# Kernel tuning notes

Measured on AMD Instinct MI355X. Metric: run time of the kernel, lower is better.

The kernel has to match this reference:

```python
import jax, jax.numpy as jnp
import numpy as np

B, T, V, C, NB, NOPS = 8, 2048, 4096, 128, 64, 8

_NONLIN = [
    lambda h: h,
    jax.nn.relu,
    lambda h: jax.nn.gelu(h, approximate=False),
    lambda h: jnp.square(h),
    lambda h: -h,
    jnp.abs,
    jnp.tanh,
    jax.nn.sigmoid,
]


def setup_inputs() -> dict:
    key = jax.random.key(0)
    ks = jax.random.split(key, 6)
    s = 0.02
    return {
        "x": jax.random.normal(ks[0], (B, T, V), dtype=jnp.float32),
        "basis": jax.random.normal(ks[1], (V, 2 * NB), dtype=jnp.float32),
        "read_coeffs": jax.random.normal(ks[2], (C, 2 * NB), dtype=jnp.float32) * s,
        "write_coeffs": jax.random.normal(ks[3], (C, 2 * NB), dtype=jnp.float32) * s,
        "op_logits": jnp.zeros((NOPS,), dtype=jnp.float32),
        "op_weights": jax.random.normal(ks[4], (NOPS, C, C), dtype=jnp.float32) * s,
        "op_biases": jnp.zeros((NOPS, C), dtype=jnp.float32),
        "out_scale": jnp.float32(0.1),
    }


def op_bank(values, op_logits, op_weights, op_biases):
    # values: (B, T, C); soft mixture of 8 small channel transforms
    w = jax.nn.softmax(op_logits)  # (n_ops,)
    result = jnp.zeros_like(values)
    for i in range(NOPS):
        h = values @ op_weights[i] + op_biases[i]
        h = _NONLIN[i % len(_NONLIN)](h)
        result = result + w[i] * h
    return result


def reference(x, basis, read_coeffs, write_coeffs, op_logits, op_weights, op_biases, out_scale):
    # READ: Fourier soft addressing over V registers, normalized over registers (axis 0)
    read_w = jax.nn.softmax(basis @ read_coeffs.T, axis=0)  # (V, C)
    values = x @ read_w  # (B, T, C)
    # SELECT OP + APPLY
    values = op_bank(values, op_logits, op_weights, op_biases)
    # WRITE: unnormalized Fourier addressing back to registers
    write_w = basis @ write_coeffs.T  # (V, C)
    return (values @ write_w.T) * out_scale  # (B, T, V)
```

## Files before the change

### kernel.cpp

```cpp
#include <hip/hip_runtime.h>
#include <math.h>

#define M_TOT 16384
#define V_DIM 4096
#define C_DIM 128

typedef __bf16 bf16;
typedef __bf16 bf16x8 __attribute__((ext_vector_type(8)));
typedef float f32x4 __attribute__((ext_vector_type(4)));

__device__ inline f32x4 zero4() { f32x4 z; z[0]=0.f; z[1]=0.f; z[2]=0.f; z[3]=0.f; return z; }

__device__ inline bf16 f2bf(float f) {
  union { float f; unsigned u; } a; a.f = f;
  unsigned r = (a.u + 0x7FFFu + ((a.u >> 16) & 1u)) >> 16;
  union { unsigned short s; bf16 b; } o; o.s = (unsigned short)r;
  return o.b;
}

__device__ inline bf16x8 cvt8(float4 a, float4 b) {
  bf16x8 r;
  r[0]=f2bf(a.x); r[1]=f2bf(a.y); r[2]=f2bf(a.z); r[3]=f2bf(a.w);
  r[4]=f2bf(b.x); r[5]=f2bf(b.y); r[6]=f2bf(b.z); r[7]=f2bf(b.w);
  return r;
}

__global__ __launch_bounds__(256) void k_read(const float* __restrict__ basis,
                                              const float* __restrict__ rc,
                                              bf16* __restrict__ RT) {
  const int c = blockIdx.x;
  const int t = threadIdx.x;
  __shared__ __align__(16) float coeff[128];
  __shared__ float logits[4096];
  __shared__ float red[256];
  if (t < 128) coeff[t] = rc[c * 128 + t];
  __syncthreads();
  float lmax = -3.0e38f;
  for (int v = t; v < V_DIM; v += 256) {
    const float4* br = (const float4*)(basis + v * 128);
    const float4* cr = (const float4*)coeff;
    float s = 0.f;
#pragma unroll 8
    for (int k = 0; k < 32; k++) {
      float4 b4 = br[k]; float4 c4 = cr[k];
      s += b4.x * c4.x; s += b4.y * c4.y; s += b4.z * c4.z; s += b4.w * c4.w;
    }
    logits[v] = s;
    lmax = fmaxf(lmax, s);
  }
  red[t] = lmax;
  __syncthreads();
  for (int off = 128; off > 0; off >>= 1) {
    if (t < off) red[t] = fmaxf(red[t], red[t + off]);
    __syncthreads();
  }
  const float gmax = red[0];
  __syncthreads();
  float lsum = 0.f;
  for (int v = t; v < V_DIM; v += 256) {
    float e = __expf(logits[v] - gmax);
    logits[v] = e;
    lsum += e;
  }
  red[t] = lsum;
  __syncthreads();
  for (int off = 128; off > 0; off >>= 1) {
    if (t < off) red[t] += red[t + off];
    __syncthreads();
  }
  const float inv = 1.f / red[0];
  for (int v = t; v < V_DIM; v += 256)
    RT[c * V_DIM + v] = f2bf(logits[v] * inv);
}

__global__ __launch_bounds__(128) void k_write(const float* __restrict__ basis,
                                               const float* __restrict__ wc,
                                               bf16* __restrict__ W2) {
  const int v = blockIdx.x;
  const int c = threadIdx.x;
  __shared__ __align__(16) float brow[128];
  brow[c] = basis[v * 128 + c];
  __syncthreads();
  const float4* cr = (const float4*)(wc + c * 128);
  const float4* br = (const float4*)brow;
  float s = 0.f;
#pragma unroll 8
  for (int k = 0; k < 32; k++) {
    float4 a = br[k], b = cr[k];
    s += a.x * b.x; s += a.y * b.y; s += a.z * b.z; s += a.w * b.w;
  }
  W2[v * 128 + c] = f2bf(s);
}

__global__ __launch_bounds__(256) void k_ops(const float* __restrict__ opw,
                                             bf16* __restrict__ WTO) {
  int idx = blockIdx.x * 256 + threadIdx.x;
  int i = idx >> 14, rem = idx & 16383, n = rem >> 7, k = rem & 127;
  WTO[idx] = f2bf(opw[(i << 14) + k * 128 + n]);
}

__global__ __launch_bounds__(256) void k_gemm1(const float* __restrict__ x,
                                               const bf16* __restrict__ RT,
                                               bf16* __restrict__ val) {
  __shared__ __align__(16) bf16 Asm[64][72];
  __shared__ __align__(16) bf16 Bsm[128][72];
  const int t = threadIdx.x;
  const int m0 = blockIdx.x * 64;
  const int lane = t & 63, wave = t >> 6;
  const int fm = lane & 15, quad = lane >> 4;

  f32x4 acc[8];
#pragma unroll
  for (int i = 0; i < 8; i++) acc[i] = zero4();

  const int ar = t >> 2, ac = (t & 3) * 16;
  const int br = t >> 1, bc = (t & 1) * 32;
  const float* xp = x + (size_t)(m0 + ar) * V_DIM + ac;
  const bf16* bp = RT + br * V_DIM + bc;

  for (int k0 = 0; k0 < V_DIM; k0 += 64) {
    float4 a0 = *(const float4*)(xp + k0);
    float4 a1 = *(const float4*)(xp + k0 + 4);
    float4 a2 = *(const float4*)(xp + k0 + 8);
    float4 a3 = *(const float4*)(xp + k0 + 12);
    uint4 b0 = *(const uint4*)(bp + k0);
    uint4 b1 = *(const uint4*)(bp + k0 + 8);
    uint4 b2 = *(const uint4*)(bp + k0 + 16);
    uint4 b3 = *(const uint4*)(bp + k0 + 24);
    __syncthreads();
    *(bf16x8*)&Asm[ar][ac]     = cvt8(a0, a1);
    *(bf16x8*)&Asm[ar][ac + 8] = cvt8(a2, a3);
    *(uint4*)&Bsm[br][bc]      = b0;
    *(uint4*)&Bsm[br][bc + 8]  = b1;
    *(uint4*)&Bsm[br][bc + 16] = b2;
    *(uint4*)&Bsm[br][bc + 24] = b3;
    __syncthreads();
    bf16x8 af0 = *(const bf16x8*)&Asm[wave * 16 + fm][quad * 8];
    bf16x8 af1 = *(const bf16x8*)&Asm[wave * 16 + fm][32 + quad * 8];
#pragma unroll
    for (int nt = 0; nt < 8; nt++) {
      bf16x8 bf0 = *(const bf16x8*)&Bsm[nt * 16 + fm][quad * 8];
      bf16x8 bf1 = *(const bf16x8*)&Bsm[nt * 16 + fm][32 + quad * 8];
      acc[nt] = __builtin_amdgcn_mfma_f32_16x16x32_bf16(af0, bf0, acc[nt], 0, 0, 0);
      acc[nt] = __builtin_amdgcn_mfma_f32_16x16x32_bf16(af1, bf1, acc[nt], 0, 0, 0);
    }
  }
#pragma unroll
  for (int nt = 0; nt < 8; nt++)
#pragma unroll
    for (int r = 0; r < 4; r++) {
      int row = m0 + wave * 16 + quad * 4 + r;
      val[row * 128 + nt * 16 + fm] = f2bf(acc[nt][r]);
    }
}

__device__ inline float apply_nonlin(int i, float v) {
  switch (i) {
    case 0: return v;
    case 1: return fmaxf(v, 0.f);
    case 2: return 0.5f * v * (1.f + erff(v * 0.70710678118654752f));
    case 3: return v * v;
    case 4: return -v;
    case 5: return fabsf(v);
    case 6: return tanhf(v);
    default: return 1.f / (1.f + __expf(-v));
  }
}

__global__ __launch_bounds__(256) void k_opbank(const bf16* __restrict__ val,
                                                const bf16* __restrict__ WTO,
                                                const float* __restrict__ op_logits,
                                                const float* __restrict__ op_biases,
                                                bf16* __restrict__ val2) {
  __shared__ __align__(16) bf16 Asm[64][136];
  __shared__ __align__(16) bf16 Bsm[128][136];
  const int t = threadIdx.x;
  const int m0 = blockIdx.x * 64;
  const int lane = t & 63, wave = t >> 6;
  const int fm = lane & 15, quad = lane >> 4;

  float w[8];
  {
    float lm = -3.0e38f;
#pragma unroll
    for (int i = 0; i < 8; i++) { w[i] = op_logits[i]; lm = fmaxf(lm, w[i]); }
    float s = 0.f;
#pragma unroll
    for (int i = 0; i < 8; i++) { w[i] = __expf(w[i] - lm); s += w[i]; }
    float inv = 1.f / s;
#pragma unroll
    for (int i = 0; i < 8; i++) w[i] *= inv;
  }

  {
    const int row = t >> 2, off = (t & 3) * 32;
    const uint4* p = (const uint4*)(val + (m0 + row) * 128 + off);
    uint4 q0 = p[0], q1 = p[1], q2 = p[2], q3 = p[3];
    uint4* d = (uint4*)&Asm[row][off];
    d[0] = q0; d[1] = q1; d[2] = q2; d[3] = q3;
  }
  __syncthreads();
  bf16x8 af[4];
#pragma unroll
  for (int kk = 0; kk < 4; kk++)
    af[kk] = *(const bf16x8*)&Asm[wave * 16 + fm][kk * 32 + quad * 8];

  f32x4 res[8];
#pragma unroll
  for (int nt = 0; nt < 8; nt++) res[nt] = zero4();

  const int brow = t >> 1, boff = (t & 1) * 64;
  for (int i = 0; i < 8; i++) {
    __syncthreads();
    {
      const uint4* p = (const uint4*)(WTO + i * 16384 + brow * 128 + boff);
      uint4* d = (uint4*)&Bsm[brow][boff];
#pragma unroll
      for (int j = 0; j < 8; j++) d[j] = p[j];
    }
    __syncthreads();
#pragma unroll
    for (int nt = 0; nt < 8; nt++) {
      f32x4 h = zero4();
#pragma unroll
      for (int kk = 0; kk < 4; kk++) {
        bf16x8 bfr = *(const bf16x8*)&Bsm[nt * 16 + fm][kk * 32 + quad * 8];
        h = __builtin_amdgcn_mfma_f32_16x16x32_bf16(af[kk], bfr, h, 0, 0, 0);
      }
      float bias = op_biases[i * 128 + nt * 16 + fm];
#pragma unroll
      for (int r = 0; r < 4; r++) {
        float vv = h[r] + bias;
        res[nt][r] += w[i] * apply_nonlin(i, vv);
      }
    }
  }
#pragma unroll
  for (int nt = 0; nt < 8; nt++)
#pragma unroll
    for (int r = 0; r < 4; r++) {
      int row = m0 + wave * 16 + quad * 4 + r;
      val2[row * 128 + nt * 16 + fm] = f2bf(res[nt][r]);
    }
}

__global__ __launch_bounds__(256) void k_gemm2(const bf16* __restrict__ val2,
                                               const bf16* __restrict__ W2,
                                               const float* __restrict__ p_scale,
                                               float* __restrict__ out) {
  __shared__ __align__(16) bf16 Asm[64][136];
  __shared__ __align__(16) bf16 Bsm[128][136];
  const int t = threadIdx.x;
  const int m0 = (blockIdx.x >> 5) * 64;
  const int n0 = (blockIdx.x & 31) * 128;
  const int lane = t & 63, wave = t >> 6;
  const int fm = lane & 15, quad = lane >> 4;

  {
    const int row = t >> 2, off = (t & 3) * 32;
    const uint4* p = (const uint4*)(val2 + (m0 + row) * 128 + off);
    uint4* d = (uint4*)&Asm[row][off];
#pragma unroll
    for (int j = 0; j < 4; j++) d[j] = p[j];
  }
  {
    const int row = t >> 1, off = (t & 1) * 64;
    const uint4* p = (const uint4*)(W2 + (n0 + row) * 128 + off);
    uint4* d = (uint4*)&Bsm[row][off];
#pragma unroll
    for (int j = 0; j < 8; j++) d[j] = p[j];
  }
  __syncthreads();

  const float scale = *p_scale;
  bf16x8 af[4];
#pragma unroll
  for (int kk = 0; kk < 4; kk++)
    af[kk] = *(const bf16x8*)&Asm[wave * 16 + fm][kk * 32 + quad * 8];

#pragma unroll
  for (int nt = 0; nt < 8; nt++) {
    f32x4 acc = zero4();
#pragma unroll
    for (int kk = 0; kk < 4; kk++) {
      bf16x8 bfr = *(const bf16x8*)&Bsm[nt * 16 + fm][kk * 32 + quad * 8];
      acc = __builtin_amdgcn_mfma_f32_16x16x32_bf16(af[kk], bfr, acc, 0, 0, 0);
    }
#pragma unroll
    for (int r = 0; r < 4; r++) {
      int row = m0 + wave * 16 + quad * 4 + r;
      out[(size_t)row * V_DIM + n0 + nt * 16 + fm] = acc[r] * scale;
    }
  }
}

extern "C" void kernel_launch(void* const* d_in, const int* in_sizes, int n_in,
                              void* d_out, int out_size, void* d_ws, size_t ws_size,
                              hipStream_t stream) {
  const float* x      = (const float*)d_in[0];
  const float* basis  = (const float*)d_in[1];
  const float* rc     = (const float*)d_in[2];
  const float* wc     = (const float*)d_in[3];
  const float* oplog  = (const float*)d_in[4];
  const float* opw    = (const float*)d_in[5];
  const float* opb    = (const float*)d_in[6];
  const float* oscale = (const float*)d_in[7];
  float* out = (float*)d_out;
  char* ws = (char*)d_ws;

  bf16* RT   = (bf16*)(ws);
  bf16* W2   = (bf16*)(ws + (1u << 20));
  bf16* WTO  = (bf16*)(ws + (2u << 20));
  bf16* VAL  = (bf16*)(ws + (2u << 20) + (1u << 19));
  bf16* VAL2 = (bf16*)(ws + (2u << 20) + (1u << 19) + (4u << 20));

  k_read <<<C_DIM, 256, 0, stream>>>(basis, rc, RT);
  k_write<<<V_DIM, 128, 0, stream>>>(basis, wc, W2);
  k_ops  <<<512, 256, 0, stream>>>(opw, WTO);
  k_gemm1<<<M_TOT / 64, 256, 0, stream>>>(x, RT, VAL);
  k_opbank<<<M_TOT / 64, 256, 0, stream>>>(VAL, WTO, oplog, opb, VAL2);
  k_gemm2<<<(M_TOT / 64) * (V_DIM / 128), 256, 0, stream>>>(VAL2, W2, oscale, out);
}
```

Baseline: 653.3 us.

## Use MFMA for addressing matmuls, split-K gemm1, and stage gemm2 stores through LDS

Replaces the scalar read/write addressing kernels with MFMA-based GEMMs plus a separate register-resident softmax. gemm1 becomes split-K over 4 chunks for 4x more blocks, and the opbank kernel sums the partials, using 32-row tiles to double its block count. gemm2 reorders blocks to walk M fastest and writes output through LDS so the global stores are coalesced float4. This costs extra partial-sum traffic and one more bf16 rounding of the partial results.

```diff
diff --git a/kernel.cpp b/kernel.cpp
--- a/kernel.cpp
+++ b/kernel.cpp
@@ -25,29 +25,71 @@
   return r;
 }
 
-__global__ __launch_bounds__(256) void k_read(const float* __restrict__ basis,
-                                              const float* __restrict__ rc,
-                                              bf16* __restrict__ RT) {
-  const int c = blockIdx.x;
+__global__ __launch_bounds__(256) void k_logits(const float* __restrict__ basis,
+                                                const float* __restrict__ rc,
+                                                float* __restrict__ LT) {
+  __shared__ __align__(16) bf16 Asm[128][136];
+  __shared__ __align__(16) bf16 Bsm[128][136];
   const int t = threadIdx.x;
-  __shared__ __align__(16) float coeff[128];
-  __shared__ float logits[4096];
+  const int v0 = blockIdx.x * 128;
+  const int lane = t & 63, wave = t >> 6, fm = lane & 15, quad = lane >> 4;
+
+  {
+    const int row = t >> 1, c0 = (t & 1) * 64;
+    const float4* p = (const float4*)(rc + row * 128 + c0);
+    bf16x8* d = (bf16x8*)&Asm[row][c0];
+#pragma unroll
+    for (int j = 0; j < 8; j++) { float4 a = p[2*j], b = p[2*j+1]; d[j] = cvt8(a, b); }
+  }
+  {
+    const int row = t >> 1, c0 = (t & 1) * 64;
+    const float4* p = (const float4*)(basis + (size_t)(v0 + row) * 128 + c0);
+    bf16x8* d = (bf16x8*)&Bsm[row][c0];
+#pragma unroll
+    for (int j = 0; j < 8; j++) { float4 a = p[2*j], b = p[2*j+1]; d[j] = cvt8(a, b); }
+  }
+  __syncthreads();
+
+  f32x4 acc[2][8];
+#pragma unroll
+  for (int m = 0; m < 2; m++)
+#pragma unroll
+    for (int n = 0; n < 8; n++) acc[m][n] = zero4();
+
+#pragma unroll
+  for (int kk = 0; kk < 4; kk++) {
+    bf16x8 af[2];
+#pragma unroll
+    for (int m = 0; m < 2; m++)
+      af[m] = *(const bf16x8*)&Asm[wave * 32 + m * 16 + fm][kk * 32 + quad * 8];
+#pragma unroll
+    for (int nt = 0; nt < 8; nt++) {
+      bf16x8 bfr = *(const bf16x8*)&Bsm[nt * 16 + fm][kk * 32 + quad * 8];
+#pragma unroll
+      for (int m = 0; m < 2; m++)
+        acc[m][nt] = __builtin_amdgcn_mfma_f32_16x16x32_bf16(af[m], bfr, acc[m][nt], 0, 0, 0);
+    }
+  }
+#pragma unroll
+  for (int m = 0; m < 2; m++)
+#pragma unroll
+    for (int nt = 0; nt < 8; nt++)
+#pragma unroll
+      for (int r = 0; r < 4; r++) {
+        int c = wave * 32 + m * 16 + quad * 4 + r;
+        LT[(size_t)c * V_DIM + v0 + nt * 16 + fm] = acc[m][nt][r];
+      }
+}
+
+__global__ __launch_bounds__(256) void k_softmax(const float* __restrict__ LT,
+                                                 bf16* __restrict__ RT) {
+  const int c = blockIdx.x, t = threadIdx.x;
   __shared__ float red[256];
-  if (t < 128) coeff[t] = rc[c * 128 + t];
-  __syncthreads();
+  const float* row = LT + (size_t)c * V_DIM;
+  float e[16];
   float lmax = -3.0e38f;
-  for (int v = t; v < V_DIM; v += 256) {
-    const float4* br = (const float4*)(basis + v * 128);
-    const float4* cr = (const float4*)coeff;
-    float s = 0.f;
-#pragma unroll 8
-    for (int k = 0; k < 32; k++) {
-      float4 b4 = br[k]; float4 c4 = cr[k];
-      s += b4.x * c4.x; s += b4.y * c4.y; s += b4.z * c4.z; s += b4.w * c4.w;
-    }
-    logits[v] = s;
-    lmax = fmaxf(lmax, s);
-  }
+#pragma unroll
+  for (int j = 0; j < 16; j++) { e[j] = row[t + 256 * j]; lmax = fmaxf(lmax, e[j]); }
   red[t] = lmax;
   __syncthreads();
   for (int off = 128; off > 0; off >>= 1) {
@@ -57,11 +99,8 @@
   const float gmax = red[0];
   __syncthreads();
   float lsum = 0.f;
-  for (int v = t; v < V_DIM; v += 256) {
-    float e = __expf(logits[v] - gmax);
-    logits[v] = e;
-    lsum += e;
-  }
+#pragma unroll
+  for (int j = 0; j < 16; j++) { e[j] = __expf(e[j] - gmax); lsum += e[j]; }
   red[t] = lsum;
   __syncthreads();
   for (int off = 128; off > 0; off >>= 1) {
@@ -69,27 +108,55 @@
     __syncthreads();
   }
   const float inv = 1.f / red[0];
-  for (int v = t; v < V_DIM; v += 256)
-    RT[c * V_DIM + v] = f2bf(logits[v] * inv);
-}
-
-__global__ __launch_bounds__(128) void k_write(const float* __restrict__ basis,
-                                               const float* __restrict__ wc,
-                                               bf16* __restrict__ W2) {
-  const int v = blockIdx.x;
-  const int c = threadIdx.x;
-  __shared__ __align__(16) float brow[128];
-  brow[c] = basis[v * 128 + c];
-  __syncthreads();
-  const float4* cr = (const float4*)(wc + c * 128);
-  const float4* br = (const float4*)brow;
-  float s = 0.f;
-#pragma unroll 8
-  for (int k = 0; k < 32; k++) {
-    float4 a = br[k], b = cr[k];
-    s += a.x * b.x; s += a.y * b.y; s += a.z * b.z; s += a.w * b.w;
-  }
-  W2[v * 128 + c] = f2bf(s);
+#pragma unroll
+  for (int j = 0; j < 16; j++)
+    RT[(size_t)c * V_DIM + t + 256 * j] = f2bf(e[j] * inv);
+}
+
+__global__ __launch_bounds__(256) void k_w2(const float* __restrict__ basis,
+                                            const float* __restrict__ wc,
+                                            bf16* __restrict__ W2) {
+  __shared__ __align__(16) bf16 Asm[64][136];
+  __shared__ __align__(16) bf16 Bsm[128][136];
+  const int t = threadIdx.x;
+  const int v0 = blockIdx.x * 64;
+  const int lane = t & 63, wave = t >> 6, fm = lane & 15, quad = lane >> 4;
+
+  {
+    const int row = t >> 2, c0 = (t & 3) * 32;
+    const float4* p = (const float4*)(basis + (size_t)(v0 + row) * 128 + c0);
+    bf16x8* d = (bf16x8*)&Asm[row][c0];
+#pragma unroll
+    for (int j = 0; j < 4; j++) { float4 a = p[2*j], b = p[2*j+1]; d[j] = cvt8(a, b); }
+  }
+  {
+    const int row = t >> 1, c0 = (t & 1) * 64;
+    const float4* p = (const float4*)(wc + row * 128 + c0);
+    bf16x8* d = (bf16x8*)&Bsm[row][c0];
+#pragma unroll
+    for (int j = 0; j < 8; j++) { float4 a = p[2*j], b = p[2*j+1]; d[j] = cvt8(a, b); }
+  }
+  __syncthreads();
+
+  f32x4 acc[8];
+#pragma unroll
+  for (int n = 0; n < 8; n++) acc[n] = zero4();
+#pragma unroll
+  for (int kk = 0; kk < 4; kk++) {
+    bf16x8 af = *(const bf16x8*)&Asm[wave * 16 + fm][kk * 32 + quad * 8];
+#pragma unroll
+    for (int nt = 0; nt < 8; nt++) {
+      bf16x8 bfr = *(const bf16x8*)&Bsm[nt * 16 + fm][kk * 32 + quad * 8];
+      acc[nt] = __builtin_amdgcn_mfma_f32_16x16x32_bf16(af, bfr, acc[nt], 0, 0, 0);
+    }
+  }
+#pragma unroll
+  for (int nt = 0; nt < 8; nt++)
+#pragma unroll
+    for (int r = 0; r < 4; r++) {
+      int v = v0 + wave * 16 + quad * 4 + r;
+      W2[v * 128 + nt * 16 + fm] = f2bf(acc[nt][r]);
+    }
 }
 
 __global__ __launch_bounds__(256) void k_ops(const float* __restrict__ opw,
@@ -101,11 +168,12 @@
 
 __global__ __launch_bounds__(256) void k_gemm1(const float* __restrict__ x,
                                                const bf16* __restrict__ RT,
-                                               bf16* __restrict__ val) {
+                                               bf16* __restrict__ PART) {
   __shared__ __align__(16) bf16 Asm[64][72];
   __shared__ __align__(16) bf16 Bsm[128][72];
   const int t = threadIdx.x;
-  const int m0 = blockIdx.x * 64;
+  const int kc = blockIdx.x & 3;
+  const int m0 = (blockIdx.x >> 2) * 64;
   const int lane = t & 63, wave = t >> 6;
   const int fm = lane & 15, quad = lane >> 4;
 
@@ -116,9 +184,10 @@
   const int ar = t >> 2, ac = (t & 3) * 16;
   const int br = t >> 1, bc = (t & 1) * 32;
   const float* xp = x + (size_t)(m0 + ar) * V_DIM + ac;
-  const bf16* bp = RT + br * V_DIM + bc;
-
-  for (int k0 = 0; k0 < V_DIM; k0 += 64) {
+  const bf16* bp = RT + (size_t)br * V_DIM + bc;
+  const int kbeg = kc * 1024, kend = kbeg + 1024;
+
+  for (int k0 = kbeg; k0 < kend; k0 += 64) {
     float4 a0 = *(const float4*)(xp + k0);
     float4 a1 = *(const float4*)(xp + k0 + 4);
     float4 a2 = *(const float4*)(xp + k0 + 8);
@@ -145,12 +214,13 @@
       acc[nt] = __builtin_amdgcn_mfma_f32_16x16x32_bf16(af1, bf1, acc[nt], 0, 0, 0);
     }
   }
+  bf16* po = PART + (size_t)kc * (M_TOT * C_DIM);
 #pragma unroll
   for (int nt = 0; nt < 8; nt++)
 #pragma unroll
     for (int r = 0; r < 4; r++) {
       int row = m0 + wave * 16 + quad * 4 + r;
-      val[row * 128 + nt * 16 + fm] = f2bf(acc[nt][r]);
+      po[row * 128 + nt * 16 + fm] = f2bf(acc[nt][r]);
     }
 }
 
@@ -167,17 +237,18 @@
   }
 }
 
-__global__ __launch_bounds__(256) void k_opbank(const bf16* __restrict__ val,
+__global__ __launch_bounds__(256) void k_opbank(const bf16* __restrict__ PART,
                                                 const bf16* __restrict__ WTO,
                                                 const float* __restrict__ op_logits,
                                                 const float* __restrict__ op_biases,
                                                 bf16* __restrict__ val2) {
-  __shared__ __align__(16) bf16 Asm[64][136];
+  __shared__ __align__(16) bf16 Asm[32][136];
   __shared__ __align__(16) bf16 Bsm[128][136];
   const int t = threadIdx.x;
-  const int m0 = blockIdx.x * 64;
+  const int m0 = blockIdx.x * 32;
   const int lane = t & 63, wave = t >> 6;
   const int fm = lane & 15, quad = lane >> 4;
+  const int mf = wave & 1, nh = wave >> 1;
 
   float w[8];
   {
@@ -193,21 +264,33 @@
   }
 
   {
-    const int row = t >> 2, off = (t & 3) * 32;
-    const uint4* p = (const uint4*)(val + (m0 + row) * 128 + off);
-    uint4 q0 = p[0], q1 = p[1], q2 = p[2], q3 = p[3];
-    uint4* d = (uint4*)&Asm[row][off];
-    d[0] = q0; d[1] = q1; d[2] = q2; d[3] = q3;
-  }
-  __syncthreads();
+    const int row = t >> 3, c0 = (t & 7) * 16;
+    float accA[16];
+#pragma unroll
+    for (int j = 0; j < 16; j++) accA[j] = 0.f;
+#pragma unroll
+    for (int p = 0; p < 4; p++) {
+      const bf16x8* q = (const bf16x8*)(PART + (size_t)p * (M_TOT * C_DIM) + (m0 + row) * 128 + c0);
+      bf16x8 u0 = q[0], u1 = q[1];
+#pragma unroll
+      for (int j = 0; j < 8; j++) { accA[j] += (float)u0[j]; accA[8 + j] += (float)u1[j]; }
+    }
+    bf16x8 o0, o1;
+#pragma unroll
+    for (int j = 0; j < 8; j++) { o0[j] = f2bf(accA[j]); o1[j] = f2bf(accA[8 + j]); }
+    *(bf16x8*)&Asm[row][c0] = o0;
+    *(bf16x8*)&Asm[row][c0 + 8] = o1;
+  }
+  __syncthreads();
+
   bf16x8 af[4];
 #pragma unroll
   for (int kk = 0; kk < 4; kk++)
-    af[kk] = *(const bf16x8*)&Asm[wave * 16 + fm][kk * 32 + quad * 8];
-
-  f32x4 res[8];
-#pragma unroll
-  for (int nt = 0; nt < 8; nt++) res[nt] = zero4();
+    af[kk] = *(const bf16x8*)&Asm[mf * 16 + fm][kk * 32 + quad * 8];
+
+  f32x4 res[4];
+#pragma unroll
+  for (int j = 0; j < 4; j++) res[j] = zero4();
 
   const int brow = t >> 1, boff = (t & 1) * 64;
   for (int i = 0; i < 8; i++) {
@@ -220,7 +303,8 @@
     }
     __syncthreads();
 #pragma unroll
-    for (int nt = 0; nt < 8; nt++) {
+    for (int j = 0; j < 4; j++) {
+      const int nt = nh * 4 + j;
       f32x4 h = zero4();
 #pragma unroll
       for (int kk = 0; kk < 4; kk++) {
@@ -231,42 +315,46 @@
 #pragma unroll
       for (int r = 0; r < 4; r++) {
         float vv = h[r] + bias;
-        res[nt][r] += w[i] * apply_nonlin(i, vv);
+        res[j][r] += w[i] * apply_nonlin(i, vv);
       }
     }
   }
 #pragma unroll
-  for (int nt = 0; nt < 8; nt++)
+  for (int j = 0; j < 4; j++) {
+    const int nt = nh * 4 + j;
 #pragma unroll
     for (int r = 0; r < 4; r++) {
-      int row = m0 + wave * 16 + quad * 4 + r;
-      val2[row * 128 + nt * 16 + fm] = f2bf(res[nt][r]);
-    }
-}
+      int row = m0 + mf * 16 + quad * 4 + r;
+      val2[row * 128 + nt * 16 + fm] = f2bf(res[j][r]);
+    }
+  }
+}
+
+struct G2S { bf16 A[64][136]; bf16 B[128][136]; };
+union G2U { G2S s; float C[64][132]; };
 
 __global__ __launch_bounds__(256) void k_gemm2(const bf16* __restrict__ val2,
                                                const bf16* __restrict__ W2,
                                                const float* __restrict__ p_scale,
                                                float* __restrict__ out) {
-  __shared__ __align__(16) bf16 Asm[64][136];
-  __shared__ __align__(16) bf16 Bsm[128][136];
+  __shared__ __align__(16) G2U u;
   const int t = threadIdx.x;
-  const int m0 = (blockIdx.x >> 5) * 64;
-  const int n0 = (blockIdx.x & 31) * 128;
+  const int n0 = (blockIdx.x >> 8) * 128;
+  const int m0 = (blockIdx.x & 255) * 64;
   const int lane = t & 63, wave = t >> 6;
   const int fm = lane & 15, quad = lane >> 4;
 
   {
     const int row = t >> 2, off = (t & 3) * 32;
     const uint4* p = (const uint4*)(val2 + (m0 + row) * 128 + off);
-    uint4* d = (uint4*)&Asm[row][off];
+    uint4* d = (uint4*)&u.s.A[row][off];
 #pragma unroll
     for (int j = 0; j < 4; j++) d[j] = p[j];
   }
   {
     const int row = t >> 1, off = (t & 1) * 64;
     const uint4* p = (const uint4*)(W2 + (n0 + row) * 128 + off);
-    uint4* d = (uint4*)&Bsm[row][off];
+    uint4* d = (uint4*)&u.s.B[row][off];
 #pragma unroll
     for (int j = 0; j < 8; j++) d[j] = p[j];
   }
@@ -276,21 +364,31 @@
   bf16x8 af[4];
 #pragma unroll
   for (int kk = 0; kk < 4; kk++)
-    af[kk] = *(const bf16x8*)&Asm[wave * 16 + fm][kk * 32 + quad * 8];
-
+    af[kk] = *(const bf16x8*)&u.s.A[wave * 16 + fm][kk * 32 + quad * 8];
+
+  f32x4 acc[8];
 #pragma unroll
   for (int nt = 0; nt < 8; nt++) {
-    f32x4 acc = zero4();
+    acc[nt] = zero4();
 #pragma unroll
     for (int kk = 0; kk < 4; kk++) {
-      bf16x8 bfr = *(const bf16x8*)&Bsm[nt * 16 + fm][kk * 32 + quad * 8];
-      acc = __builtin_amdgcn_mfma_f32_16x16x32_bf16(af[kk], bfr, acc, 0, 0, 0);
-    }
-#pragma unroll
-    for (int r = 0; r < 4; r++) {
-      int row = m0 + wave * 16 + quad * 4 + r;
-      out[(size_t)row * V_DIM + n0 + nt * 16 + fm] = acc[r] * scale;
-    }
+      bf16x8 bfr = *(const bf16x8*)&u.s.B[nt * 16 + fm][kk * 32 + quad * 8];
+      acc[nt] = __builtin_amdgcn_mfma_f32_16x16x32_bf16(af[kk], bfr, acc[nt], 0, 0, 0);
+    }
+  }
+  __syncthreads();
+#pragma unroll
+  for (int nt = 0; nt < 8; nt++)
+#pragma unroll
+    for (int r = 0; r < 4; r++)
+      u.C[wave * 16 + quad * 4 + r][nt * 16 + fm] = acc[nt][r] * scale;
+  __syncthreads();
+#pragma unroll
+  for (int j = 0; j < 8; j++) {
+    int idx = t + 256 * j;
+    int row = idx >> 5, c4 = idx & 31;
+    float4 v = *(const float4*)&u.C[row][c4 * 4];
+    *(float4*)(out + (size_t)(m0 + row) * V_DIM + n0 + c4 * 4) = v;
   }
 }
 
@@ -308,16 +406,18 @@
   float* out = (float*)d_out;
   char* ws = (char*)d_ws;
 
-  bf16* RT   = (bf16*)(ws);
-  bf16* W2   = (bf16*)(ws + (1u << 20));
-  bf16* WTO  = (bf16*)(ws + (2u << 20));
-  bf16* VAL  = (bf16*)(ws + (2u << 20) + (1u << 19));
-  bf16* VAL2 = (bf16*)(ws + (2u << 20) + (1u << 19) + (4u << 20));
-
-  k_read <<<C_DIM, 256, 0, stream>>>(basis, rc, RT);
-  k_write<<<V_DIM, 128, 0, stream>>>(basis, wc, W2);
-  k_ops  <<<512, 256, 0, stream>>>(opw, WTO);
-  k_gemm1<<<M_TOT / 64, 256, 0, stream>>>(x, RT, VAL);
-  k_opbank<<<M_TOT / 64, 256, 0, stream>>>(VAL, WTO, oplog, opb, VAL2);
-  k_gemm2<<<(M_TOT / 64) * (V_DIM / 128), 256, 0, stream>>>(VAL2, W2, oscale, out);
-}
+  float* LT  = (float*)(ws);
+  bf16* RT   = (bf16*)(ws + 2097152);
+  bf16* W2   = (bf16*)(ws + 3145728);
+  bf16* WTO  = (bf16*)(ws + 4194304);
+  bf16* PART = (bf16*)(ws + 4456448);
+  bf16* VAL2 = (bf16*)(ws + 21233664);
+
+  k_logits <<<V_DIM / 128, 256, 0, stream>>>(basis, rc, LT);
+  k_w2     <<<V_DIM / 64, 256, 0, stream>>>(basis, wc, W2);
+  k_ops    <<<512, 256, 0, stream>>>(opw, WTO);
+  k_softmax<<<C_DIM, 256, 0, stream>>>(LT, RT);
+  k_gemm1  <<<(M_TOT / 64) * 4, 256, 0, stream>>>(x, RT, PART);
+  k_opbank <<<M_TOT / 32, 256, 0, stream>>>(PART, WTO, oplog, opb, VAL2);
+  k_gemm2  <<<(M_TOT / 64) * (V_DIM / 128), 256, 0, stream>>>(VAL2, W2, oscale, out);
+}
```

Measured after the change: 582.6 us. 1.12x faster.
